# Optimization experiments

Hardware: AMD Instinct MI355X
Metric: run time of the kernel (lower is better)

The kernel has to match this reference:

```python
import jax, jax.numpy as jnp
import numpy as np

D_MODEL = 1024
N_HEADS = 16
D_HEAD = D_MODEL // N_HEADS
B, T = 2, 2048


def setup_inputs() -> dict:
    key = jax.random.key(0)
    k1, k2, k3 = jax.random.split(key, 3)
    x = jax.random.normal(k1, (B, T, D_MODEL), dtype=jnp.float32)
    # torch nn.Linear weights: y = x @ W.T, W has shape [out, in]
    W_qkv = jax.random.normal(k2, (3 * D_MODEL, D_MODEL), dtype=jnp.float32) * (1.0 / np.sqrt(D_MODEL))
    W_out = jax.random.normal(k3, (D_MODEL, D_MODEL), dtype=jnp.float32) * (1.0 / np.sqrt(D_MODEL))
    return {"x": x, "W_qkv": W_qkv, "W_out": W_out}


def reference(x, W_qkv, W_out):
    Bb, Tt, Dd = x.shape
    qkv = (x @ W_qkv.T).reshape(Bb, Tt, 3, N_HEADS, D_HEAD)
    q, k, v = qkv[:, :, 0], qkv[:, :, 1], qkv[:, :, 2]  # [B,T,H,d]
    q = q.transpose(0, 2, 1, 3)  # [B,H,T,d]
    k = k.transpose(0, 2, 1, 3)
    v = v.transpose(0, 2, 1, 3)
    scale = 1.0 / np.sqrt(D_HEAD)
    scores = jnp.einsum('bhqd,bhkd->bhqk', q, k) * scale  # [B,H,T,T]
    causal = jnp.tril(jnp.ones((Tt, Tt), dtype=bool))
    scores = jnp.where(causal, scores, -jnp.inf)
    A = jax.nn.softmax(scores, axis=-1)
    AV = jnp.einsum('bhqk,bhkd->bhqd', A, v)
    AAV = jnp.einsum('bhqk,bhkd->bhqd', A, AV)  # twicing correction
    out = 2.0 * AV - AAV  # [B,H,T,d]
    out = out.transpose(0, 2, 1, 3).reshape(Bb, Tt, Dd)
    return out @ W_out.T
```

## Files before the change

### kernel.cpp

```cpp
#include <hip/hip_runtime.h>
#include <hip/hip_bf16.h>

#define T_SEQ  2048
#define DMODEL 1024
#define NH     16
#define DH     64
#define NTOK   4096
#define QSCALE 0.18033688011112042f
#define M_FIX  16.0f

typedef unsigned short u16;
typedef short s16x8 __attribute__((ext_vector_type(8)));
typedef unsigned short u16x8 __attribute__((ext_vector_type(8)));
typedef float f32x4 __attribute__((ext_vector_type(4)));

__device__ __forceinline__ u16 f2bf(float f) {
  unsigned u = __float_as_uint(f);
  u += 0x7FFFu + ((u >> 16) & 1u);
  return (u16)(u >> 16);
}
__device__ __forceinline__ unsigned pk2(float a, float b) {
  __hip_bfloat162 h = __float22bfloat162_rn(make_float2(a, b));
  unsigned u;
  __builtin_memcpy(&u, &h, 4);
  return u;
}
__device__ __forceinline__ unsigned pk2z(float a, float b) {
  return __builtin_amdgcn_perm(__float_as_uint(b), __float_as_uint(a), 0x07060302);
}
__device__ __forceinline__ float bf2f(u16 x) {
  return __uint_as_float(((unsigned)x) << 16);
}
__device__ __forceinline__ void async_cp16(const u16* g, u16* l) {
  __builtin_amdgcn_global_load_lds(
      (const __attribute__((address_space(1))) unsigned*)g,
      (__attribute__((address_space(3))) unsigned*)l, 16, 0, 0);
}

__global__ void cast_to_bf16(const float* __restrict__ in, u16* __restrict__ out, int n4) {
  int i = blockIdx.x * blockDim.x + threadIdx.x;
  if (i >= n4) return;
  float4 v = reinterpret_cast<const float4*>(in)[i];
  ushort4 r;
  r.x = f2bf(v.x); r.y = f2bf(v.y); r.z = f2bf(v.z); r.w = f2bf(v.w);
  reinterpret_cast<ushort4*>(out)[i] = r;
}

__global__ __launch_bounds__(512, 2) void gemm_qkv(
    const u16* __restrict__ A, const u16* __restrict__ Bm,
    u16* __restrict__ outQ, u16* __restrict__ outK, u16* __restrict__ outV) {
  __shared__ __align__(16) u16 SM[65536];
  const int tid = threadIdx.x, wave = tid >> 6, lane = tid & 63;
  const int f15 = lane & 15, quad = lane >> 4;
  const int bm = blockIdx.x * 256, bn = blockIdx.y * 256;
  const int wm = wave >> 2, wn = wave & 3;
  const int K = DMODEL;

  f32x4 acc[8][4] = {};

  const u16* Ag0 = A  + (size_t)(bm + (2 * wave) * 16 + f15) * K + quad * 8;
  const u16* Ag1 = A  + (size_t)(bm + (2 * wave + 1) * 16 + f15) * K + quad * 8;
  const u16* Bg0 = Bm + (size_t)(bn + (2 * wave) * 16 + f15) * K + quad * 8;
  const u16* Bg1 = Bm + (size_t)(bn + (2 * wave + 1) * 16 + f15) * K + quad * 8;
  u16* LA0 = SM + (2 * wave) * 512 + lane * 8;
  u16* LA1 = SM + (2 * wave + 1) * 512 + lane * 8;
  u16* LB0 = SM + 8192 + (2 * wave) * 512 + lane * 8;
  u16* LB1 = SM + 8192 + (2 * wave + 1) * 512 + lane * 8;

  const int S = K >> 5;
#pragma unroll
  for (int s = 0; s < 3; s++) {
    const int k0 = s * 32, o = s * 16384;
    async_cp16(Ag0 + k0, LA0 + o); async_cp16(Ag1 + k0, LA1 + o);
    async_cp16(Bg0 + k0, LB0 + o); async_cp16(Bg1 + k0, LB1 + o);
  }

  for (int s = 0; s < S; s++) {
    if (s < S - 2)       asm volatile("s_waitcnt vmcnt(8)" ::: "memory");
    else if (s == S - 2) asm volatile("s_waitcnt vmcnt(4)" ::: "memory");
    else                 asm volatile("s_waitcnt vmcnt(0)" ::: "memory");
    __builtin_amdgcn_s_barrier();
    __builtin_amdgcn_sched_barrier(0);
    if (s + 3 < S) {
      const int k0 = (s + 3) * 32, o = ((s + 3) & 3) * 16384;
      async_cp16(Ag0 + k0, LA0 + o); async_cp16(Ag1 + k0, LA1 + o);
      async_cp16(Bg0 + k0, LB0 + o); async_cp16(Bg1 + k0, LB1 + o);
    }
    const u16* Sl = SM + (s & 3) * 16384;
    s16x8 af[8], bfr[4];
#pragma unroll
    for (int ni = 0; ni < 4; ni++)
      bfr[ni] = *reinterpret_cast<const s16x8*>(Sl + 8192 + (wn * 4 + ni) * 512 + lane * 8);
#pragma unroll
    for (int mi = 0; mi < 8; mi++)
      af[mi] = *reinterpret_cast<const s16x8*>(Sl + (wm * 8 + mi) * 512 + lane * 8);
    __builtin_amdgcn_s_setprio(1);
#pragma unroll
    for (int mi = 0; mi < 8; mi++)
#pragma unroll
      for (int ni = 0; ni < 4; ni++)
        acc[mi][ni] = __builtin_amdgcn_mfma_f32_16x16x32_bf16(af[mi], bfr[ni], acc[mi][ni], 0, 0, 0);
    __builtin_amdgcn_s_setprio(0);
  }

  __syncthreads();
  u16* Cs = SM;
  const int ST = 264;
  if (bn < 2048) {
    const float scale = (bn < 1024) ? QSCALE : 1.0f;
#pragma unroll
    for (int c = 0; c < 4; c++) {
      if (c) __syncthreads();
      if (wm == (c >> 1)) {
#pragma unroll
        for (int mi2 = 0; mi2 < 4; mi2++) {
          const int mi = (c & 1) * 4 + mi2;
#pragma unroll
          for (int ni = 0; ni < 4; ni++) {
            const int col = (wn * 4 + ni) * 16 + f15;
#pragma unroll
            for (int r = 0; r < 4; r++)
              Cs[(mi2 * 16 + quad * 4 + r) * ST + col] = f2bf(acc[mi][ni][r] * scale);
          }
        }
      }
      __syncthreads();
      const int row = tid >> 3, cb = (tid & 7) * 32;
      const int gm = bm + c * 64 + row;
#pragma unroll
      for (int c8 = 0; c8 < 4; c8++) {
        const int gc = bn + cb + c8 * 8;
        u16x8 v = *reinterpret_cast<const u16x8*>(&Cs[row * ST + cb + c8 * 8]);
        const int which = gc >> 10, hh = (gc >> 6) & 15, d = gc & 63;
        u16* dst = (which ? outK : outQ) + ((size_t)hh * NTOK + gm) * 64 + d;
        *reinterpret_cast<u16x8*>(dst) = v;
      }
    }
  } else {
    const int bnV = bn - 2048;
#pragma unroll
    for (int c = 0; c < 4; c++) {
      if (c) __syncthreads();
      if (wm == (c >> 1)) {
#pragma unroll
        for (int mi2 = 0; mi2 < 4; mi2++) {
          const int mi = (c & 1) * 4 + mi2;
#pragma unroll
          for (int ni = 0; ni < 4; ni++) {
            const int col = (wn * 4 + ni) * 16 + f15;
#pragma unroll
            for (int r = 0; r < 4; r++)
              Cs[(mi2 * 16 + quad * 4 + r) * ST + col] = f2bf(acc[mi][ni][r]);
          }
        }
      }
      __syncthreads();
      const int fc = tid >> 3, s8 = (tid & 7) * 8;
      const int tb = ((s8 >> 5) & 1) * 32 + ((s8 >> 3) & 3) * 4;
      const int gmb = bm + c * 64;
#pragma unroll
      for (int p = 0; p < 4; p++) {
        const int d = p * 64 + fc;
        u16x8 vv;
#pragma unroll
        for (int j = 0; j < 4; j++) vv[j] = Cs[(tb + j) * ST + d];
#pragma unroll
        for (int j = 0; j < 4; j++) vv[4 + j] = Cs[(tb + 16 + j) * ST + d];
        *reinterpret_cast<u16x8*>(outV + (size_t)(bnV + d) * NTOK + gmb + s8) = vv;
      }
    }
  }
}

__global__ __launch_bounds__(256) void gemm_out(
    const u16* __restrict__ A, const u16* __restrict__ Bm, float* __restrict__ outF) {
  __shared__ __align__(16) u16 SM[18432];
  const int tid = threadIdx.x, wave = tid >> 6, lane = tid & 63;
  const int f15 = lane & 15, quad = lane >> 4;
  const int bm = blockIdx.x * 64, bn = blockIdx.y * 128;
  const int wr = wave >> 1, wc = wave & 1;
  const int K = DMODEL, N = DMODEL;

  f32x4 acc[2][4] = {};

  const u16* Ag = A  + (size_t)(bm + wave * 16 + f15) * K + quad * 8;
  const u16* Bg0 = Bm + (size_t)(bn + (2 * wave) * 16 + f15) * K + quad * 8;
  const u16* Bg1 = Bm + (size_t)(bn + (2 * wave + 1) * 16 + f15) * K + quad * 8;
  u16* LA  = SM + wave * 512 + lane * 8;
  u16* LB0 = SM + 2048 + (2 * wave) * 512 + lane * 8;
  u16* LB1 = SM + 2048 + (2 * wave + 1) * 512 + lane * 8;

  const int KT = K >> 5;
  async_cp16(Ag, LA); async_cp16(Bg0, LB0); async_cp16(Bg1, LB1);
  async_cp16(Ag + 32, LA + 6144); async_cp16(Bg0 + 32, LB0 + 6144); async_cp16(Bg1 + 32, LB1 + 6144);

  int bufr = 0, bufw = 2;
  for (int kt = 0; kt < KT; kt++) {
    if (kt + 1 < KT) asm volatile("s_waitcnt vmcnt(3)" ::: "memory");
    else             asm volatile("s_waitcnt vmcnt(0)" ::: "memory");
    __builtin_amdgcn_s_barrier();
    __builtin_amdgcn_sched_barrier(0);
    if (kt + 2 < KT) {
      const int k0 = (kt + 2) * 32;
      const int o = bufw * 6144;
      async_cp16(Ag + k0, LA + o); async_cp16(Bg0 + k0, LB0 + o); async_cp16(Bg1 + k0, LB1 + o);
    }
    const u16* Af = SM + bufr * 6144;
    const u16* Bf = Af + 2048;
    s16x8 af[2], bfr[4];
#pragma unroll
    for (int mi = 0; mi < 2; mi++)
      af[mi] = *reinterpret_cast<const s16x8*>(Af + (wr * 2 + mi) * 512 + lane * 8);
#pragma unroll
    for (int ni = 0; ni < 4; ni++)
      bfr[ni] = *reinterpret_cast<const s16x8*>(Bf + (wc * 4 + ni) * 512 + lane * 8);
#pragma unroll
    for (int mi = 0; mi < 2; mi++)
#pragma unroll
      for (int ni = 0; ni < 4; ni++)
        acc[mi][ni] = __builtin_amdgcn_mfma_f32_16x16x32_bf16(af[mi], bfr[ni], acc[mi][ni], 0, 0, 0);
    bufr = (bufr == 2) ? 0 : bufr + 1;
    bufw = (bufw == 2) ? 0 : bufw + 1;
  }

#pragma unroll
  for (int mi = 0; mi < 2; mi++)
#pragma unroll
    for (int ni = 0; ni < 4; ni++)
#pragma unroll
      for (int r = 0; r < 4; r++)
        outF[(size_t)(bm + wr * 32 + mi * 16 + quad * 4 + r) * N + bn + wc * 64 + ni * 16 + f15] =
            acc[mi][ni][r];
}

template <int PASS>
__global__ __launch_bounds__(256) void attn_pass(
    const u16* __restrict__ Qb, const u16* __restrict__ Kb, const u16* __restrict__ Vsrc,
    float* __restrict__ LinvG, u16* __restrict__ Vp2, u16* __restrict__ TW) {
  __shared__ __align__(16) u16 SM[16384];
  const int tid = threadIdx.x, wave = tid >> 6, lane = tid & 63;
  const int f15 = lane & 15, quad = lane >> 4;
  const int bid = blockIdx.x;
  const int y = (bid & 7) * 4 + ((bid >> 3) & 3);
  const int b = y >> 4, h = y & 15;
  const int g = bid >> 5, a = g & 7;
  const int gq = g >> 3;
  const int qt = (gq == 0) ? (31 - a) : (gq == 1) ? (8 + a) : (gq == 2) ? (23 - a) : a;
  const int q0 = qt * 64;
  const int ntiles = qt + 1;
  const size_t qk_base = ((size_t)h * NTOK + (size_t)b * T_SEQ) * 64;
  const size_t vt_base = (size_t)h * 64 * NTOK + (size_t)b * T_SEQ;

  const int qw = q0 + 16 * wave;
  s16x8 qf0, qf1;
  {
    const u16* qp = Qb + qk_base + (size_t)(qw + f15) * 64 + quad * 8;
    qf0 = *reinterpret_cast<const s16x8*>(qp);
    qf1 = *reinterpret_cast<const s16x8*>(qp + 32);
  }
  float invl_r = 0.f;
  if (PASS == 1) invl_r = LinvG[(size_t)y * T_SEQ + qw + f15];

  f32x4 accO[4] = {};
  float l_acc = 0.f;

  const u16* Kg = Kb  + qk_base + (size_t)(wave * 16 + f15) * 64 + quad * 8;
  const u16* Vg = Vsrc + vt_base + (size_t)(wave * 16 + f15) * NTOK + quad * 8;
  u16* LK = SM + (wave * 2) * 512 + lane * 8;
  u16* LV = SM + 4096 + (wave * 2) * 512 + lane * 8;

  async_cp16(Kg, LK); async_cp16(Kg + 32, LK + 512);
  async_cp16(Vg, LV); async_cp16(Vg + 32, LV + 512);
  __syncthreads();

  for (int ti = 0; ti < ntiles; ti++) {
    const int buf = ti & 1;
    if (ti + 1 < ntiles) {
      const int j1 = (ti + 1) * 64;
      const int o = (buf ^ 1) * 8192;
      async_cp16(Kg + (size_t)j1 * 64, LK + o);
      async_cp16(Kg + (size_t)j1 * 64 + 32, LK + o + 512);
      async_cp16(Vg + j1, LV + o);
      async_cp16(Vg + j1 + 32, LV + o + 512);
    }
    const u16* Kf = SM + buf * 8192;
    const u16* Vf = SM + buf * 8192 + 4096;

    f32x4 accS[4] = {};
#pragma unroll
    for (int st = 0; st < 4; st++) {
      s16x8 k0 = *reinterpret_cast<const s16x8*>(Kf + (st * 2) * 512 + lane * 8);
      s16x8 k1 = *reinterpret_cast<const s16x8*>(Kf + (st * 2 + 1) * 512 + lane * 8);
      accS[st] = __builtin_amdgcn_mfma_f32_16x16x32_bf16(k0, qf0, accS[st], 0, 0, 0);
      accS[st] = __builtin_amdgcn_mfma_f32_16x16x32_bf16(k1, qf1, accS[st], 0, 0, 0);
    }
    union pbu { s16x8 v; unsigned u[4]; } pb0, pb1;
    if (ti < qt) {
#pragma unroll
      for (int st = 0; st < 4; st++) {
        float e0 = __builtin_amdgcn_exp2f(accS[st][0] - M_FIX);
        float e1 = __builtin_amdgcn_exp2f(accS[st][1] - M_FIX);
        float e2 = __builtin_amdgcn_exp2f(accS[st][2] - M_FIX);
        float e3 = __builtin_amdgcn_exp2f(accS[st][3] - M_FIX);
        if (PASS == 0) l_acc += (e0 + e1) + (e2 + e3);
        unsigned w0 = pk2z(e0, e1), w1 = pk2z(e2, e3);
        if (st < 2) { pb0.u[(st & 1) * 2] = w0; pb0.u[(st & 1) * 2 + 1] = w1; }
        else        { pb1.u[(st & 1) * 2] = w0; pb1.u[(st & 1) * 2 + 1] = w1; }
      }
    } else {
      const int qrel = 16 * wave + f15;
#pragma unroll
      for (int st = 0; st < 4; st++) {
        const int jb = st * 16 + quad * 4;
        float e0 = (jb + 0 <= qrel) ? __builtin_amdgcn_exp2f(accS[st][0] - M_FIX) : 0.f;
        float e1 = (jb + 1 <= qrel) ? __builtin_amdgcn_exp2f(accS[st][1] - M_FIX) : 0.f;
        float e2 = (jb + 2 <= qrel) ? __builtin_amdgcn_exp2f(accS[st][2] - M_FIX) : 0.f;
        float e3 = (jb + 3 <= qrel) ? __builtin_amdgcn_exp2f(accS[st][3] - M_FIX) : 0.f;
        if (PASS == 0) l_acc += (e0 + e1) + (e2 + e3);
        unsigned w0 = pk2z(e0, e1), w1 = pk2z(e2, e3);
        if (st < 2) { pb0.u[(st & 1) * 2] = w0; pb0.u[(st & 1) * 2 + 1] = w1; }
        else        { pb1.u[(st & 1) * 2] = w0; pb1.u[(st & 1) * 2 + 1] = w1; }
      }
    }
#pragma unroll
    for (int mt = 0; mt < 4; mt++) {
      s16x8 v0 = *reinterpret_cast<const s16x8*>(Vf + (mt * 2) * 512 + lane * 8);
      s16x8 v1 = *reinterpret_cast<const s16x8*>(Vf + (mt * 2 + 1) * 512 + lane * 8);
      accO[mt] = __builtin_amdgcn_mfma_f32_16x16x32_bf16(v0, pb0.v, accO[mt], 0, 0, 0);
      accO[mt] = __builtin_amdgcn_mfma_f32_16x16x32_bf16(v1, pb1.v, accO[mt], 0, 0, 0);
    }
    __syncthreads();
  }

  if (PASS == 0) {
    float l = l_acc;
    l += __shfl_xor(l, 16);
    l += __shfl_xor(l, 32);
    invl_r = 1.0f / l;
    if (quad == 0) LinvG[(size_t)y * T_SEQ + qw + f15] = invl_r;
  }

  if (PASS == 0) {
    u16* E = SM;
    const int ql = 16 * wave + f15;
    const int slot = (ql >> 5) * 32 + ((ql >> 2) & 3) * 8 + ((ql >> 4) & 1) * 4 + (ql & 3);
#pragma unroll
    for (int mt = 0; mt < 4; mt++)
#pragma unroll
      for (int r = 0; r < 4; r++)
        E[(mt * 16 + quad * 4 + r) * 68 + slot] = f2bf(accO[mt][r] * invl_r);
    __syncthreads();
    const int d = tid >> 2, s = (tid & 3) * 16;
    const u16* vg2 = Vsrc + vt_base + (size_t)d * NTOK + q0 + s;
    u16* og = Vp2 + vt_base + (size_t)d * NTOK + q0 + s;
#pragma unroll
    for (int g2 = 0; g2 < 2; g2++) {
      u16x8 vv = *reinterpret_cast<const u16x8*>(vg2 + g2 * 8);
      u16x8 ee = *reinterpret_cast<const u16x8*>(&E[d * 68 + s + g2 * 8]);
      u16x8 oo;
#pragma unroll
      for (int i = 0; i < 8; i++) oo[i] = f2bf(2.0f * bf2f(vv[i]) - bf2f(ee[i]));
      *reinterpret_cast<u16x8*>(og + g2 * 8) = oo;
    }
  } else {
    u16* E2 = SM;
#pragma unroll
    for (int mt = 0; mt < 4; mt++) {
      uint2 w;
      w.x = pk2(accO[mt][0] * invl_r, accO[mt][1] * invl_r);
      w.y = pk2(accO[mt][2] * invl_r, accO[mt][3] * invl_r);
      *reinterpret_cast<uint2*>(&E2[(16 * wave + f15) * 72 + mt * 16 + quad * 4]) = w;
    }
    __syncthreads();
    const int q = tid >> 2, s = (tid & 3) * 16;
    u16* dst = TW + ((size_t)b * T_SEQ + q0 + q) * DMODEL + h * 64 + s;
    *reinterpret_cast<u16x8*>(dst) = *reinterpret_cast<const u16x8*>(&E2[q * 72 + s]);
    *reinterpret_cast<u16x8*>(dst + 8) = *reinterpret_cast<const u16x8*>(&E2[q * 72 + s + 8]);
  }
}

extern "C" void kernel_launch(void* const* d_in, const int* in_sizes, int n_in,
                              void* d_out, int out_size, void* d_ws, size_t ws_size,
                              hipStream_t stream) {
  const float* x    = (const float*)d_in[0];
  const float* Wqkv = (const float*)d_in[1];
  const float* Wout = (const float*)d_in[2];
  float* out = (float*)d_out;
  char* ws = (char*)d_ws;

  u16*   Xb    = (u16*)(ws + 0);
  u16*   Wqkvb = (u16*)(ws + 8388608);
  u16*   Woutb = (u16*)(ws + 14680064);
  u16*   Qb    = (u16*)(ws + 16777216);
  u16*   Kb    = (u16*)(ws + 25165824);
  u16*   Vtp   = (u16*)(ws + 33554432);
  u16*   TW    = (u16*)(ws + 41943040);
  u16*   Vp2   = (u16*)(ws + 50331648);
  float* LinvG = (float*)(ws + 58720256);

  cast_to_bf16<<<4096, 256, 0, stream>>>(x, Xb, 1048576);
  cast_to_bf16<<<3072, 256, 0, stream>>>(Wqkv, Wqkvb, 786432);
  cast_to_bf16<<<1024, 256, 0, stream>>>(Wout, Woutb, 262144);

  gemm_qkv<<<dim3(16, 12), 512, 0, stream>>>(Xb, Wqkvb, Qb, Kb, Vtp);

  attn_pass<0><<<1024, 256, 0, stream>>>(Qb, Kb, Vtp, LinvG, Vp2, nullptr);
  attn_pass<1><<<1024, 256, 0, stream>>>(Qb, Kb, Vp2, LinvG, nullptr, TW);

  gemm_out<<<dim3(64, 8), 256, 0, stream>>>(TW, Woutb, out);
}
```

Before: 222.7 us.

## Double-buffer QKV GEMM LDS fragments in registers and merge cast kernels

The QKV GEMM main loop is unrolled by two, with two register sets of A/B fragments. LDS reads for the next k-step are issued before the MFMAs of the current one, so shared-memory latency overlaps with matrix-core work. The three fp32-to-bf16 cast launches are merged into one kernel that relies on the workspace buffers being contiguous, which removes two launches. The cost is extra register pressure from the second fragment set and more intricate waitcnt and barrier ordering.

```diff
diff --git a/kernel.cpp b/kernel.cpp
--- a/kernel.cpp
+++ b/kernel.cpp
@@ -37,14 +37,38 @@
       (__attribute__((address_space(3))) unsigned*)l, 16, 0, 0);
 }
 
-__global__ void cast_to_bf16(const float* __restrict__ in, u16* __restrict__ out, int n4) {
+__global__ void cast_all(const float* __restrict__ x, const float* __restrict__ wqkv,
+                         const float* __restrict__ wout, u16* __restrict__ out) {
   int i = blockIdx.x * blockDim.x + threadIdx.x;
-  if (i >= n4) return;
-  float4 v = reinterpret_cast<const float4*>(in)[i];
+  const float* src; int off;
+  if (i < 1048576)      { src = x;    off = 0; }
+  else if (i < 1835008) { src = wqkv; off = 1048576; }
+  else                  { src = wout; off = 1835008; }
+  float4 v = reinterpret_cast<const float4*>(src)[i - off];
   ushort4 r;
   r.x = f2bf(v.x); r.y = f2bf(v.y); r.z = f2bf(v.z); r.w = f2bf(v.w);
   reinterpret_cast<ushort4*>(out)[i] = r;
 }
+
+#define QKV_STAGE(s_) do { \
+    const int k0_ = (s_) * 32, o_ = ((s_) & 3) * 16384; \
+    async_cp16(Ag0 + k0_, LA0 + o_); async_cp16(Ag1 + k0_, LA1 + o_); \
+    async_cp16(Bg0 + k0_, LB0 + o_); async_cp16(Bg1 + k0_, LB1 + o_); \
+  } while (0)
+#define QKV_LOAD(slotbase_, af_, bf_) do { \
+    const u16* Sl_ = (slotbase_); \
+    _Pragma("unroll") for (int ni_ = 0; ni_ < 4; ni_++) \
+      bf_[ni_] = *reinterpret_cast<const s16x8*>(Sl_ + 8192 + (wn * 4 + ni_) * 512 + lane * 8); \
+    _Pragma("unroll") for (int mi_ = 0; mi_ < 8; mi_++) \
+      af_[mi_] = *reinterpret_cast<const s16x8*>(Sl_ + (wm * 8 + mi_) * 512 + lane * 8); \
+  } while (0)
+#define QKV_MFMA(af_, bf_) do { \
+    __builtin_amdgcn_s_setprio(1); \
+    _Pragma("unroll") for (int mi_ = 0; mi_ < 8; mi_++) \
+      _Pragma("unroll") for (int ni_ = 0; ni_ < 4; ni_++) \
+        acc[mi_][ni_] = __builtin_amdgcn_mfma_f32_16x16x32_bf16(af_[mi_], bf_[ni_], acc[mi_][ni_], 0, 0, 0); \
+    __builtin_amdgcn_s_setprio(0); \
+  } while (0)
 
 __global__ __launch_bounds__(512, 2) void gemm_qkv(
     const u16* __restrict__ A, const u16* __restrict__ Bm,
@@ -68,39 +92,33 @@
   u16* LB1 = SM + 8192 + (2 * wave + 1) * 512 + lane * 8;
 
   const int S = K >> 5;
-#pragma unroll
-  for (int s = 0; s < 3; s++) {
-    const int k0 = s * 32, o = s * 16384;
-    async_cp16(Ag0 + k0, LA0 + o); async_cp16(Ag1 + k0, LA1 + o);
-    async_cp16(Bg0 + k0, LB0 + o); async_cp16(Bg1 + k0, LB1 + o);
-  }
-
-  for (int s = 0; s < S; s++) {
-    if (s < S - 2)       asm volatile("s_waitcnt vmcnt(8)" ::: "memory");
-    else if (s == S - 2) asm volatile("s_waitcnt vmcnt(4)" ::: "memory");
-    else                 asm volatile("s_waitcnt vmcnt(0)" ::: "memory");
+  s16x8 afA[8], bfA[4], afB[8], bfB[4];
+
+  QKV_STAGE(0); QKV_STAGE(1); QKV_STAGE(2);
+  asm volatile("s_waitcnt vmcnt(8)" ::: "memory");
+  __builtin_amdgcn_s_barrier();
+  __builtin_amdgcn_sched_barrier(0);
+  QKV_LOAD(SM, afA, bfA);
+
+  for (int s = 0; s < S; s += 2) {
+    if (s + 2 < S) asm volatile("s_waitcnt vmcnt(4)" ::: "memory");
+    else           asm volatile("s_waitcnt vmcnt(0)" ::: "memory");
     __builtin_amdgcn_s_barrier();
     __builtin_amdgcn_sched_barrier(0);
-    if (s + 3 < S) {
-      const int k0 = (s + 3) * 32, o = ((s + 3) & 3) * 16384;
-      async_cp16(Ag0 + k0, LA0 + o); async_cp16(Ag1 + k0, LA1 + o);
-      async_cp16(Bg0 + k0, LB0 + o); async_cp16(Bg1 + k0, LB1 + o);
-    }
-    const u16* Sl = SM + (s & 3) * 16384;
-    s16x8 af[8], bfr[4];
-#pragma unroll
-    for (int ni = 0; ni < 4; ni++)
-      bfr[ni] = *reinterpret_cast<const s16x8*>(Sl + 8192 + (wn * 4 + ni) * 512 + lane * 8);
-#pragma unroll
-    for (int mi = 0; mi < 8; mi++)
-      af[mi] = *reinterpret_cast<const s16x8*>(Sl + (wm * 8 + mi) * 512 + lane * 8);
-    __builtin_amdgcn_s_setprio(1);
-#pragma unroll
-    for (int mi = 0; mi < 8; mi++)
-#pragma unroll
-      for (int ni = 0; ni < 4; ni++)
-        acc[mi][ni] = __builtin_amdgcn_mfma_f32_16x16x32_bf16(af[mi], bfr[ni], acc[mi][ni], 0, 0, 0);
-    __builtin_amdgcn_s_setprio(0);
+    if (s + 3 < S) QKV_STAGE(s + 3);
+    QKV_LOAD(SM + ((s + 1) & 3) * 16384, afB, bfB);
+    QKV_MFMA(afA, bfA);
+    if (s + 2 < S) {
+      if (s + 3 < S) asm volatile("s_waitcnt vmcnt(4)" ::: "memory");
+      else           asm volatile("s_waitcnt vmcnt(0)" ::: "memory");
+      __builtin_amdgcn_s_barrier();
+      __builtin_amdgcn_sched_barrier(0);
+      if (s + 4 < S) QKV_STAGE(s + 4);
+      QKV_LOAD(SM + ((s + 2) & 3) * 16384, afA, bfA);
+      QKV_MFMA(afB, bfB);
+    } else {
+      QKV_MFMA(afB, bfB);
+    }
   }
 
   __syncthreads();
@@ -398,9 +416,7 @@
   u16*   Vp2   = (u16*)(ws + 50331648);
   float* LinvG = (float*)(ws + 58720256);
 
-  cast_to_bf16<<<4096, 256, 0, stream>>>(x, Xb, 1048576);
-  cast_to_bf16<<<3072, 256, 0, stream>>>(Wqkv, Wqkvb, 786432);
-  cast_to_bf16<<<1024, 256, 0, stream>>>(Wout, Woutb, 262144);
+  cast_all<<<8192, 256, 0, stream>>>(x, Wqkv, Wout, Xb);
 
   gemm_qkv<<<dim3(16, 12), 512, 0, stream>>>(Xb, Wqkvb, Qb, Kb, Vtp);
 
```

Result: slower. 476.3 us (+113.9%).

## Double attention query tile per block and fuse bf16 casts into one kernel

Applied to the files above, without the earlier changes.

Each attention block now handles 128 query rows instead of 64, with every wave owning two 16-row query groups that share each K/V tile loaded into LDS. This halves the K/V traffic per query row and halves the grid to 512 blocks, with per-wave skipping of fully masked tiles. The epilogue writes out in two 64-row halves with extra barriers. The three input cast kernels are merged into one launch over contiguous workspace buffers. The cost is more registers per wave (doubled accumulators) and fewer blocks, which may hurt occupancy and load balance.

```diff
diff --git a/kernel.cpp b/kernel.cpp
--- a/kernel.cpp
+++ b/kernel.cpp
@@ -37,10 +37,14 @@
       (__attribute__((address_space(3))) unsigned*)l, 16, 0, 0);
 }
 
-__global__ void cast_to_bf16(const float* __restrict__ in, u16* __restrict__ out, int n4) {
+__global__ void cast_all(const float* __restrict__ x, const float* __restrict__ wqkv,
+                         const float* __restrict__ wout, u16* __restrict__ out) {
   int i = blockIdx.x * blockDim.x + threadIdx.x;
-  if (i >= n4) return;
-  float4 v = reinterpret_cast<const float4*>(in)[i];
+  const float* src; int off;
+  if (i < 1048576)      { src = x;    off = 0; }
+  else if (i < 1835008) { src = wqkv; off = 1048576; }
+  else                  { src = wout; off = 1835008; }
+  float4 v = reinterpret_cast<const float4*>(src)[i - off];
   ushort4 r;
   r.x = f2bf(v.x); r.y = f2bf(v.y); r.z = f2bf(v.z); r.w = f2bf(v.w);
   reinterpret_cast<ushort4*>(out)[i] = r;
@@ -243,26 +247,29 @@
   const int bid = blockIdx.x;
   const int y = (bid & 7) * 4 + ((bid >> 3) & 3);
   const int b = y >> 4, h = y & 15;
-  const int g = bid >> 5, a = g & 7;
-  const int gq = g >> 3;
-  const int qt = (gq == 0) ? (31 - a) : (gq == 1) ? (8 + a) : (gq == 2) ? (23 - a) : a;
-  const int q0 = qt * 64;
-  const int ntiles = qt + 1;
+  const int g = bid >> 5;
+  const int qt2 = (g < 8) ? (15 - g) : (g - 8);
+  const int q0 = qt2 * 128;
+  const int ntiles = 2 * qt2 + 2;
   const size_t qk_base = ((size_t)h * NTOK + (size_t)b * T_SEQ) * 64;
   const size_t vt_base = (size_t)h * 64 * NTOK + (size_t)b * T_SEQ;
 
-  const int qw = q0 + 16 * wave;
-  s16x8 qf0, qf1;
-  {
-    const u16* qp = Qb + qk_base + (size_t)(qw + f15) * 64 + quad * 8;
-    qf0 = *reinterpret_cast<const s16x8*>(qp);
-    qf1 = *reinterpret_cast<const s16x8*>(qp + 32);
-  }
-  float invl_r = 0.f;
-  if (PASS == 1) invl_r = LinvG[(size_t)y * T_SEQ + qw + f15];
-
-  f32x4 accO[4] = {};
-  float l_acc = 0.f;
+  s16x8 qf[2][2];
+#pragma unroll
+  for (int grp = 0; grp < 2; grp++) {
+    const u16* qp = Qb + qk_base + (size_t)(q0 + 32 * wave + 16 * grp + f15) * 64 + quad * 8;
+    qf[grp][0] = *reinterpret_cast<const s16x8*>(qp);
+    qf[grp][1] = *reinterpret_cast<const s16x8*>(qp + 32);
+  }
+  float invl[2] = {0.f, 0.f};
+  if (PASS == 1) {
+#pragma unroll
+    for (int grp = 0; grp < 2; grp++)
+      invl[grp] = LinvG[(size_t)y * T_SEQ + q0 + 32 * wave + 16 * grp + f15];
+  }
+
+  f32x4 accO[2][4] = {};
+  float l_acc[2] = {0.f, 0.f};
 
   const u16* Kg = Kb  + qk_base + (size_t)(wave * 16 + f15) * 64 + quad * 8;
   const u16* Vg = Vsrc + vt_base + (size_t)(wave * 16 + f15) * NTOK + quad * 8;
@@ -285,97 +292,133 @@
     }
     const u16* Kf = SM + buf * 8192;
     const u16* Vf = SM + buf * 8192 + 4096;
-
-    f32x4 accS[4] = {};
-#pragma unroll
-    for (int st = 0; st < 4; st++) {
-      s16x8 k0 = *reinterpret_cast<const s16x8*>(Kf + (st * 2) * 512 + lane * 8);
-      s16x8 k1 = *reinterpret_cast<const s16x8*>(Kf + (st * 2 + 1) * 512 + lane * 8);
-      accS[st] = __builtin_amdgcn_mfma_f32_16x16x32_bf16(k0, qf0, accS[st], 0, 0, 0);
-      accS[st] = __builtin_amdgcn_mfma_f32_16x16x32_bf16(k1, qf1, accS[st], 0, 0, 0);
-    }
-    union pbu { s16x8 v; unsigned u[4]; } pb0, pb1;
-    if (ti < qt) {
+    const int D = (ti - 2 * qt2) * 64;
+
+    if (D < 32 * wave + 32) {
+      f32x4 accS[2][4] = {};
 #pragma unroll
       for (int st = 0; st < 4; st++) {
-        float e0 = __builtin_amdgcn_exp2f(accS[st][0] - M_FIX);
-        float e1 = __builtin_amdgcn_exp2f(accS[st][1] - M_FIX);
-        float e2 = __builtin_amdgcn_exp2f(accS[st][2] - M_FIX);
-        float e3 = __builtin_amdgcn_exp2f(accS[st][3] - M_FIX);
-        if (PASS == 0) l_acc += (e0 + e1) + (e2 + e3);
-        unsigned w0 = pk2z(e0, e1), w1 = pk2z(e2, e3);
-        if (st < 2) { pb0.u[(st & 1) * 2] = w0; pb0.u[(st & 1) * 2 + 1] = w1; }
-        else        { pb1.u[(st & 1) * 2] = w0; pb1.u[(st & 1) * 2 + 1] = w1; }
-      }
-    } else {
-      const int qrel = 16 * wave + f15;
-#pragma unroll
-      for (int st = 0; st < 4; st++) {
-        const int jb = st * 16 + quad * 4;
-        float e0 = (jb + 0 <= qrel) ? __builtin_amdgcn_exp2f(accS[st][0] - M_FIX) : 0.f;
-        float e1 = (jb + 1 <= qrel) ? __builtin_amdgcn_exp2f(accS[st][1] - M_FIX) : 0.f;
-        float e2 = (jb + 2 <= qrel) ? __builtin_amdgcn_exp2f(accS[st][2] - M_FIX) : 0.f;
-        float e3 = (jb + 3 <= qrel) ? __builtin_amdgcn_exp2f(accS[st][3] - M_FIX) : 0.f;
-        if (PASS == 0) l_acc += (e0 + e1) + (e2 + e3);
-        unsigned w0 = pk2z(e0, e1), w1 = pk2z(e2, e3);
-        if (st < 2) { pb0.u[(st & 1) * 2] = w0; pb0.u[(st & 1) * 2 + 1] = w1; }
-        else        { pb1.u[(st & 1) * 2] = w0; pb1.u[(st & 1) * 2 + 1] = w1; }
-      }
-    }
-#pragma unroll
-    for (int mt = 0; mt < 4; mt++) {
-      s16x8 v0 = *reinterpret_cast<const s16x8*>(Vf + (mt * 2) * 512 + lane * 8);
-      s16x8 v1 = *reinterpret_cast<const s16x8*>(Vf + (mt * 2 + 1) * 512 + lane * 8);
-      accO[mt] = __builtin_amdgcn_mfma_f32_16x16x32_bf16(v0, pb0.v, accO[mt], 0, 0, 0);
-      accO[mt] = __builtin_amdgcn_mfma_f32_16x16x32_bf16(v1, pb1.v, accO[mt], 0, 0, 0);
+        s16x8 k0 = *reinterpret_cast<const s16x8*>(Kf + (st * 2) * 512 + lane * 8);
+        s16x8 k1 = *reinterpret_cast<const s16x8*>(Kf + (st * 2 + 1) * 512 + lane * 8);
+#pragma unroll
+        for (int grp = 0; grp < 2; grp++) {
+          accS[grp][st] = __builtin_amdgcn_mfma_f32_16x16x32_bf16(k0, qf[grp][0], accS[grp][st], 0, 0, 0);
+          accS[grp][st] = __builtin_amdgcn_mfma_f32_16x16x32_bf16(k1, qf[grp][1], accS[grp][st], 0, 0, 0);
+        }
+      }
+      union pbu { s16x8 v; unsigned u[4]; } pb[2][2];
+      if (D + 63 <= 32 * wave) {
+#pragma unroll
+        for (int grp = 0; grp < 2; grp++)
+#pragma unroll
+          for (int st = 0; st < 4; st++) {
+            float e0 = __builtin_amdgcn_exp2f(accS[grp][st][0] - M_FIX);
+            float e1 = __builtin_amdgcn_exp2f(accS[grp][st][1] - M_FIX);
+            float e2 = __builtin_amdgcn_exp2f(accS[grp][st][2] - M_FIX);
+            float e3 = __builtin_amdgcn_exp2f(accS[grp][st][3] - M_FIX);
+            if (PASS == 0) l_acc[grp] += (e0 + e1) + (e2 + e3);
+            unsigned w0 = pk2z(e0, e1), w1 = pk2z(e2, e3);
+            if (st < 2) { pb[grp][0].u[(st & 1) * 2] = w0; pb[grp][0].u[(st & 1) * 2 + 1] = w1; }
+            else        { pb[grp][1].u[(st & 1) * 2] = w0; pb[grp][1].u[(st & 1) * 2 + 1] = w1; }
+          }
+      } else {
+#pragma unroll
+        for (int grp = 0; grp < 2; grp++) {
+          const int qrel = 32 * wave + 16 * grp + f15;
+#pragma unroll
+          for (int st = 0; st < 4; st++) {
+            const int jb = D + st * 16 + quad * 4;
+            float e0 = (jb + 0 <= qrel) ? __builtin_amdgcn_exp2f(accS[grp][st][0] - M_FIX) : 0.f;
+            float e1 = (jb + 1 <= qrel) ? __builtin_amdgcn_exp2f(accS[grp][st][1] - M_FIX) : 0.f;
+            float e2 = (jb + 2 <= qrel) ? __builtin_amdgcn_exp2f(accS[grp][st][2] - M_FIX) : 0.f;
+            float e3 = (jb + 3 <= qrel) ? __builtin_amdgcn_exp2f(accS[grp][st][3] - M_FIX) : 0.f;
+            if (PASS == 0) l_acc[grp] += (e0 + e1) + (e2 + e3);
+            unsigned w0 = pk2z(e0, e1), w1 = pk2z(e2, e3);
+            if (st < 2) { pb[grp][0].u[(st & 1) * 2] = w0; pb[grp][0].u[(st & 1) * 2 + 1] = w1; }
+            else        { pb[grp][1].u[(st & 1) * 2] = w0; pb[grp][1].u[(st & 1) * 2 + 1] = w1; }
+          }
+        }
+      }
+#pragma unroll
+      for (int mt = 0; mt < 4; mt++) {
+        s16x8 v0 = *reinterpret_cast<const s16x8*>(Vf + (mt * 2) * 512 + lane * 8);
+        s16x8 v1 = *reinterpret_cast<const s16x8*>(Vf + (mt * 2 + 1) * 512 + lane * 8);
+#pragma unroll
+        for (int grp = 0; grp < 2; grp++) {
+          accO[grp][mt] = __builtin_amdgcn_mfma_f32_16x16x32_bf16(v0, pb[grp][0].v, accO[grp][mt], 0, 0, 0);
+          accO[grp][mt] = __builtin_amdgcn_mfma_f32_16x16x32_bf16(v1, pb[grp][1].v, accO[grp][mt], 0, 0, 0);
+        }
+      }
     }
     __syncthreads();
   }
 
   if (PASS == 0) {
-    float l = l_acc;
-    l += __shfl_xor(l, 16);
-    l += __shfl_xor(l, 32);
-    invl_r = 1.0f / l;
-    if (quad == 0) LinvG[(size_t)y * T_SEQ + qw + f15] = invl_r;
+#pragma unroll
+    for (int grp = 0; grp < 2; grp++) {
+      float l = l_acc[grp];
+      l += __shfl_xor(l, 16);
+      l += __shfl_xor(l, 32);
+      invl[grp] = 1.0f / l;
+      if (quad == 0) LinvG[(size_t)y * T_SEQ + q0 + 32 * wave + 16 * grp + f15] = invl[grp];
+    }
   }
 
   if (PASS == 0) {
     u16* E = SM;
-    const int ql = 16 * wave + f15;
-    const int slot = (ql >> 5) * 32 + ((ql >> 2) & 3) * 8 + ((ql >> 4) & 1) * 4 + (ql & 3);
-#pragma unroll
-    for (int mt = 0; mt < 4; mt++)
-#pragma unroll
-      for (int r = 0; r < 4; r++)
-        E[(mt * 16 + quad * 4 + r) * 68 + slot] = f2bf(accO[mt][r] * invl_r);
-    __syncthreads();
-    const int d = tid >> 2, s = (tid & 3) * 16;
-    const u16* vg2 = Vsrc + vt_base + (size_t)d * NTOK + q0 + s;
-    u16* og = Vp2 + vt_base + (size_t)d * NTOK + q0 + s;
-#pragma unroll
-    for (int g2 = 0; g2 < 2; g2++) {
-      u16x8 vv = *reinterpret_cast<const u16x8*>(vg2 + g2 * 8);
-      u16x8 ee = *reinterpret_cast<const u16x8*>(&E[d * 68 + s + g2 * 8]);
-      u16x8 oo;
-#pragma unroll
-      for (int i = 0; i < 8; i++) oo[i] = f2bf(2.0f * bf2f(vv[i]) - bf2f(ee[i]));
-      *reinterpret_cast<u16x8*>(og + g2 * 8) = oo;
+#pragma unroll
+    for (int g64 = 0; g64 < 2; g64++) {
+      __syncthreads();
+      if ((wave >> 1) == g64) {
+#pragma unroll
+        for (int grp = 0; grp < 2; grp++) {
+          const int ql = 32 * (wave & 1) + 16 * grp + f15;
+          const int slot = (ql >> 5) * 32 + ((ql >> 2) & 3) * 8 + ((ql >> 4) & 1) * 4 + (ql & 3);
+#pragma unroll
+          for (int mt = 0; mt < 4; mt++)
+#pragma unroll
+            for (int r = 0; r < 4; r++)
+              E[(mt * 16 + quad * 4 + r) * 68 + slot] = f2bf(accO[grp][mt][r] * invl[grp]);
+        }
+      }
+      __syncthreads();
+      const int d = tid >> 2, s = (tid & 3) * 16;
+      const u16* vg2 = Vsrc + vt_base + (size_t)d * NTOK + q0 + 64 * g64 + s;
+      u16* og = Vp2 + vt_base + (size_t)d * NTOK + q0 + 64 * g64 + s;
+#pragma unroll
+      for (int g2 = 0; g2 < 2; g2++) {
+        u16x8 vv = *reinterpret_cast<const u16x8*>(vg2 + g2 * 8);
+        u16x8 ee = *reinterpret_cast<const u16x8*>(&E[d * 68 + s + g2 * 8]);
+        u16x8 oo;
+#pragma unroll
+        for (int i = 0; i < 8; i++) oo[i] = f2bf(2.0f * bf2f(vv[i]) - bf2f(ee[i]));
+        *reinterpret_cast<u16x8*>(og + g2 * 8) = oo;
+      }
     }
   } else {
     u16* E2 = SM;
 #pragma unroll
-    for (int mt = 0; mt < 4; mt++) {
-      uint2 w;
-      w.x = pk2(accO[mt][0] * invl_r, accO[mt][1] * invl_r);
-      w.y = pk2(accO[mt][2] * invl_r, accO[mt][3] * invl_r);
-      *reinterpret_cast<uint2*>(&E2[(16 * wave + f15) * 72 + mt * 16 + quad * 4]) = w;
-    }
-    __syncthreads();
-    const int q = tid >> 2, s = (tid & 3) * 16;
-    u16* dst = TW + ((size_t)b * T_SEQ + q0 + q) * DMODEL + h * 64 + s;
-    *reinterpret_cast<u16x8*>(dst) = *reinterpret_cast<const u16x8*>(&E2[q * 72 + s]);
-    *reinterpret_cast<u16x8*>(dst + 8) = *reinterpret_cast<const u16x8*>(&E2[q * 72 + s + 8]);
+    for (int g64 = 0; g64 < 2; g64++) {
+      __syncthreads();
+      if ((wave >> 1) == g64) {
+#pragma unroll
+        for (int grp = 0; grp < 2; grp++) {
+          const int ql = 32 * (wave & 1) + 16 * grp + f15;
+#pragma unroll
+          for (int mt = 0; mt < 4; mt++) {
+            uint2 w;
+            w.x = pk2(accO[grp][mt][0] * invl[grp], accO[grp][mt][1] * invl[grp]);
+            w.y = pk2(accO[grp][mt][2] * invl[grp], accO[grp][mt][3] * invl[grp]);
+            *reinterpret_cast<uint2*>(&E2[ql * 72 + mt * 16 + quad * 4]) = w;
+          }
+        }
+      }
+      __syncthreads();
+      const int q = tid >> 2, s = (tid & 3) * 16;
+      u16* dst = TW + ((size_t)b * T_SEQ + q0 + 64 * g64 + q) * DMODEL + h * 64 + s;
+      *reinterpret_cast<u16x8*>(dst) = *reinterpret_cast<const u16x8*>(&E2[q * 72 + s]);
+      *reinterpret_cast<u16x8*>(dst + 8) = *reinterpret_cast<const u16x8*>(&E2[q * 72 + s + 8]);
+    }
   }
 }
 
@@ -398,14 +441,12 @@
   u16*   Vp2   = (u16*)(ws + 50331648);
   float* LinvG = (float*)(ws + 58720256);
 
-  cast_to_bf16<<<4096, 256, 0, stream>>>(x, Xb, 1048576);
-  cast_to_bf16<<<3072, 256, 0, stream>>>(Wqkv, Wqkvb, 786432);
-  cast_to_bf16<<<1024, 256, 0, stream>>>(Wout, Woutb, 262144);
+  cast_all<<<8192, 256, 0, stream>>>(x, Wqkv, Wout, Xb);
 
   gemm_qkv<<<dim3(16, 12), 512, 0, stream>>>(Xb, Wqkvb, Qb, Kb, Vtp);
 
-  attn_pass<0><<<1024, 256, 0, stream>>>(Qb, Kb, Vtp, LinvG, Vp2, nullptr);
-  attn_pass<1><<<1024, 256, 0, stream>>>(Qb, Kb, Vp2, LinvG, nullptr, TW);
+  attn_pass<0><<<512, 256, 0, stream>>>(Qb, Kb, Vtp, LinvG, Vp2, nullptr);
+  attn_pass<1><<<512, 256, 0, stream>>>(Qb, Kb, Vp2, LinvG, nullptr, TW);
 
   gemm_out<<<dim3(64, 8), 256, 0, stream>>>(TW, Woutb, out);
 }
```

Measured after the change: 220.6 us. No clear change (-1.0%).
